# Performance work log

Hardware: AMD Instinct MI355X
Metric: run time of the kernel (lower is better)

Reference implementation:

```python
import jax, jax.numpy as jnp
import numpy as np

EPS = 1e-5
GROUPS = 32

def group_norm(x, w, b):
    B, C, H, W = x.shape
    g = GROUPS
    xr = x.reshape(B, g, C // g, H * W)
    mean = xr.mean(axis=(2, 3), keepdims=True)
    var = xr.var(axis=(2, 3), keepdims=True)
    h = ((xr - mean) / jnp.sqrt(var + EPS)).reshape(B, C, H, W)
    return h * w[None, :, None, None] + b[None, :, None, None]

def setup_inputs() -> dict:
    key = jax.random.key(0)
    ks = jax.random.split(key, 7)
    B, C, H, W = 8, 256, 64, 64
    d = C // 8  # 32
    x = jax.random.normal(ks[0], (B, C, H, W), dtype=jnp.float32)
    norm_w = 1.0 + 0.1 * jax.random.normal(ks[1], (C,), dtype=jnp.float32)
    norm_b = 0.1 * jax.random.normal(ks[2], (C,), dtype=jnp.float32)
    s = 1.0 / np.sqrt(C)
    Wq = jax.random.normal(ks[3], (d, C), dtype=jnp.float32) * s
    Wk = jax.random.normal(ks[4], (d, C), dtype=jnp.float32) * s
    Wv = jax.random.normal(ks[5], (C, C), dtype=jnp.float32) * s
    Wproj = jax.random.normal(ks[6], (C, C), dtype=jnp.float32) * s
    gamma = jnp.full((1,), 0.5, dtype=jnp.float32)  # torch init is 0; nonzero so attention path contributes
    return {"x": x, "norm_w": norm_w, "norm_b": norm_b, "Wq": Wq, "Wk": Wk,
            "Wv": Wv, "Wproj": Wproj, "gamma": gamma}

def reference(x, norm_w, norm_b, Wq, Wk, Wv, Wproj, gamma):
    B, C, H, W = x.shape
    N = H * W
    h = group_norm(x, norm_w, norm_b)           # (B,C,H,W)
    hf = h.reshape(B, C, N)                      # flatten spatial
    d = Wq.shape[0]
    q = jnp.einsum('dc,bcn->bnd', Wq, hf)        # (B,N,d)
    k = jnp.einsum('dc,bcn->bdn', Wk, hf)        # (B,d,N)
    v = jnp.einsum('oc,bcn->bno', Wv, hf)        # (B,N,C)
    scale = d ** (-0.5)
    attn = jax.nn.softmax(jnp.einsum('bnd,bdm->bnm', q, k) * scale, axis=-1)  # (B,N,N)
    out = jnp.einsum('bnm,bmo->bno', attn, v)    # (B,N,C)
    out = out.transpose(0, 2, 1).reshape(B, C, H, W)
    proj = jnp.einsum('oc,bchw->bohw', Wproj, out)
    return x + gamma[0] * proj
```

## Files before the change

kernel.cpp:

```cpp
#include <hip/hip_runtime.h>
#include <cstdint>


typedef __bf16 bf16x8 __attribute__((ext_vector_type(8)));
typedef float f32x4 __attribute__((ext_vector_type(4)));
typedef float f32x16 __attribute__((ext_vector_type(16)));
typedef unsigned int u32x4 __attribute__((ext_vector_type(4)));
typedef unsigned short u16x4 __attribute__((ext_vector_type(4)));
typedef unsigned short u16x8 __attribute__((ext_vector_type(8)));

#define DEVI __device__ __forceinline__

DEVI unsigned short f2bf(float f) {
    __bf16 h = (__bf16)f;
    return __builtin_bit_cast(unsigned short, h);
}
DEVI float bf2f(unsigned short u) {
    unsigned int x = ((unsigned int)u) << 16;
    return __builtin_bit_cast(float, x);
}

DEVI f32x4 mfma16(bf16x8 a, bf16x8 b, f32x4 c) {
    return __builtin_amdgcn_mfma_f32_16x16x32_bf16(a, b, c, 0, 0, 0);
}
DEVI f32x16 mfma32(bf16x8 a, bf16x8 b, f32x16 c) {
    return __builtin_amdgcn_mfma_f32_32x32x16_bf16(a, b, c, 0, 0, 0);
}

DEVI void glds16(const unsigned short* g, unsigned short* l) {
    const __attribute__((address_space(1))) unsigned int* gp =
        reinterpret_cast<const __attribute__((address_space(1))) unsigned int*>(
            reinterpret_cast<uintptr_t>(g));
    __attribute__((address_space(3))) unsigned int* lp =
        reinterpret_cast<__attribute__((address_space(3))) unsigned int*>(
            reinterpret_cast<uintptr_t>(l));
    __builtin_amdgcn_global_load_lds(gp, lp, 16, 0, 0);
}

DEVI void barrier_raw() {
    asm volatile("" ::: "memory");
    __builtin_amdgcn_s_barrier();
    asm volatile("" ::: "memory");
}
DEVI void wait_vm0() {
    __builtin_amdgcn_s_waitcnt(0x3F70);
}

#define QSCALE 0.2550663133f
#define MFIX   12.0f

__global__ __launch_bounds__(256) void k_pack(
        const float* __restrict__ wq, const float* __restrict__ wk,
        const float* __restrict__ wv, const float* __restrict__ wp,
        unsigned short* __restrict__ bqk, unsigned short* __restrict__ bv,
        unsigned short* __restrict__ bp) {
    int i = blockIdx.x * 256 + threadIdx.x;
    if (i < 8192)       bqk[i] = f2bf(wq[i] * QSCALE);
    else if (i < 16384) bqk[i] = f2bf(wk[i - 8192]);
    bv[i] = f2bf(wv[i]);
    bp[i] = f2bf(wp[i]);
}

__global__ __launch_bounds__(1024) void k_gnorm(
        const float* __restrict__ x, const float* __restrict__ gw,
        const float* __restrict__ gb, unsigned short* __restrict__ ht) {
    int bg = blockIdx.x;
    int b = bg >> 5, g = bg & 31;
    const float* xb = x + ((size_t)(b * 256 + g * 8)) * 4096;
    int t = threadIdx.x;
    float s1 = 0.f, s2 = 0.f;
    const f32x4* xv4 = (const f32x4*)xb;
    for (int i = t; i < 8192; i += 1024) {
        f32x4 v = xv4[i];
        #pragma unroll
        for (int j = 0; j < 4; j++) { s1 += v[j]; s2 += v[j] * v[j]; }
    }
    #pragma unroll
    for (int off = 1; off < 64; off <<= 1) {
        s1 += __shfl_xor(s1, off);
        s2 += __shfl_xor(s2, off);
    }
    __shared__ float red[34];
    int wv_ = t >> 6;
    if ((t & 63) == 0) { red[wv_ * 2] = s1; red[wv_ * 2 + 1] = s2; }
    __syncthreads();
    if (t == 0) {
        float a = 0.f, q = 0.f;
        #pragma unroll
        for (int i = 0; i < 16; i++) { a += red[i * 2]; q += red[i * 2 + 1]; }
        float mean = a * (1.f / 32768.f);
        float var = q * (1.f / 32768.f) - mean * mean;
        red[32] = mean; red[33] = rsqrtf(var + 1e-5f);
    }
    __syncthreads();
    float mean = red[32], rstd = red[33];
    float wv8[8], bv8[8];
    #pragma unroll
    for (int c = 0; c < 8; c++) { wv8[c] = gw[g * 8 + c] * rstd; bv8[c] = gb[g * 8 + c] - mean * rstd * gw[g * 8 + c]; }
    int n0 = t * 4;
    f32x4 cv[8];
    #pragma unroll
    for (int c = 0; c < 8; c++) cv[c] = *(const f32x4*)(xb + c * 4096 + n0);
    #pragma unroll
    for (int j = 0; j < 4; j++) {
        u16x8 pk;
        #pragma unroll
        for (int c = 0; c < 8; c++) pk[c] = f2bf(cv[c][j] * wv8[c] + bv8[c]);
        *(u16x8*)(&ht[((size_t)(b * 4096 + n0 + j)) * 256 + g * 8]) = pk;
    }
}

template <int EPI>
__global__ __launch_bounds__(256) void k_gemm(
        const unsigned short* __restrict__ A, const unsigned short* __restrict__ Bw,
        void* __restrict__ outp, const float* __restrict__ xres,
        const float* __restrict__ gamma, int ldout) {
    __shared__ unsigned short lA[128 * 72];
    __shared__ unsigned short lB[64 * 72];
    int t = threadIdx.x;
    int m0 = blockIdx.x * 128, n0 = blockIdx.y * 64;
    int w = t >> 6, lane = t & 63, l15 = lane & 15, quad = lane >> 4;
    f32x4 z4 = {0.f, 0.f, 0.f, 0.f};
    f32x4 acc[2][4];
    #pragma unroll
    for (int i = 0; i < 2; i++)
        #pragma unroll
        for (int j = 0; j < 4; j++) acc[i][j] = z4;

    for (int kb = 0; kb < 4; kb++) {
        #pragma unroll
        for (int i = 0; i < 4; i++) {
            int ch = i * 256 + t;
            int row = ch >> 3, col = (ch & 7) * 8;
            u32x4 v = *(const u32x4*)(A + (size_t)(m0 + row) * 256 + kb * 64 + col);
            *(u32x4*)(&lA[row * 72 + col]) = v;
        }
        #pragma unroll
        for (int i = 0; i < 2; i++) {
            int ch = i * 256 + t;
            int row = ch >> 3, col = (ch & 7) * 8;
            u32x4 v = *(const u32x4*)(Bw + (size_t)(n0 + row) * 256 + kb * 64 + col);
            *(u32x4*)(&lB[row * 72 + col]) = v;
        }
        __syncthreads();
        #pragma unroll
        for (int ks = 0; ks < 2; ks++) {
            bf16x8 af[2], bfr[4];
            #pragma unroll
            for (int fr = 0; fr < 2; fr++)
                af[fr] = *(const bf16x8*)(&lA[(w * 32 + fr * 16 + l15) * 72 + ks * 32 + quad * 8]);
            #pragma unroll
            for (int fn = 0; fn < 4; fn++)
                bfr[fn] = *(const bf16x8*)(&lB[(fn * 16 + l15) * 72 + ks * 32 + quad * 8]);
            #pragma unroll
            for (int fr = 0; fr < 2; fr++)
                #pragma unroll
                for (int fn = 0; fn < 4; fn++)
                    acc[fr][fn] = mfma16(af[fr], bfr[fn], acc[fr][fn]);
        }
        __syncthreads();
    }

    if (EPI == 0) {
        unsigned short* out = (unsigned short*)outp;
        #pragma unroll
        for (int fr = 0; fr < 2; fr++)
            #pragma unroll
            for (int fn = 0; fn < 4; fn++)
                #pragma unroll
                for (int r = 0; r < 4; r++) {
                    int m = m0 + w * 32 + fr * 16 + quad * 4 + r;
                    int n = n0 + fn * 16 + l15;
                    out[(size_t)m * ldout + n] = f2bf(acc[fr][fn][r]);
                }
    } else if (EPI == 1) {
        unsigned short* out = (unsigned short*)outp;
        int b = m0 >> 12, nb = (m0 & 4095) + w * 32;
        int swq = ((quad & 1) << 1) | (quad >> 1);
        #pragma unroll
        for (int fr = 0; fr < 2; fr++)
            #pragma unroll
            for (int fn = 0; fn < 4; fn++) {
                int o = n0 + fn * 16 + l15;
                int n = nb + fr * 16 + swq * 4;
                u16x4 pk;
                #pragma unroll
                for (int r = 0; r < 4; r++) pk[r] = f2bf(acc[fr][fn][r]);
                *(u16x4*)(&out[(((size_t)(b * 256 + o)) << 12) + n]) = pk;
            }
    } else {
        float* out = (float*)outp;
        float gm = gamma[0];
        int b = m0 >> 12, nb = (m0 & 4095) + w * 32;
        #pragma unroll
        for (int fr = 0; fr < 2; fr++)
            #pragma unroll
            for (int fn = 0; fn < 4; fn++) {
                int o = n0 + fn * 16 + l15;
                int n = nb + fr * 16 + quad * 4;
                size_t base = (((size_t)(b * 256 + o)) << 12) + n;
                f32x4 xv = *(const f32x4*)(xres + base);
                f32x4 ov;
                #pragma unroll
                for (int r = 0; r < 4; r++) ov[r] = xv[r] + gm * acc[fr][fn][r];
                *(f32x4*)(out + base) = ov;
            }
    }
}

__global__ __launch_bounds__(256, 2) void k_flash(
        const unsigned short* __restrict__ QK, const unsigned short* __restrict__ Vt,
        unsigned short* __restrict__ Oa) {
    __shared__ __align__(16) char smem[73728];
    int id = blockIdx.x;
    int b = id & 7, qt = id >> 3;
    int t = threadIdx.x, w = t >> 6, ln = t & 63;
    int l31 = ln & 31, h = ln >> 5;
    int qh = w >> 1, kh = w & 1;
    int q0 = qt * 64;

    const unsigned short* qrow = QK + ((size_t)(b * 4096 + q0 + qh * 32 + l31)) * 64;
    bf16x8 qb0 = *(const bf16x8*)(qrow + h * 8);
    bf16x8 qb1 = *(const bf16x8*)(qrow + 16 + h * 8);

    int cgK = (ln & 3) ^ ((ln >> 2) & 3) ^ ((ln >> 4) & 3);
    const unsigned short* gK = QK + ((size_t)(b * 4096 + w * 16 + (ln >> 2))) * 64 + 32 + cgK * 8;
    int vc8 = (ln & 7) ^ ((ln >> 3) & 7);
    const unsigned short* gV = Vt + (((size_t)(b * 256 + w * 64 + (ln >> 3))) << 12) + vc8 * 8;

    unsigned short* lK0 = (unsigned short*)smem;
    unsigned short* lV0 = (unsigned short*)(smem + 4096);
    unsigned short* lK1 = (unsigned short*)(smem + 36864);
    unsigned short* lV1 = (unsigned short*)(smem + 36864 + 4096);
    unsigned short* sK0 = lK0 + w * 512;
    unsigned short* sV0 = lV0 + w * 4096;
    unsigned short* sK1 = lK1 + w * 512;
    unsigned short* sV1 = lV1 + w * 4096;

    u16x8 onesu = {0x3F80, 0x3F80, 0x3F80, 0x3F80, 0x3F80, 0x3F80, 0x3F80, 0x3F80};
    bf16x8 ones = __builtin_bit_cast(bf16x8, onesu);
    f32x16 z16;
    #pragma unroll
    for (int i = 0; i < 16; i++) z16[i] = 0.f;
    f32x16 minit;
    #pragma unroll
    for (int i = 0; i < 16; i++) minit[i] = -MFIX;
    f32x16 Oacc[8];
    #pragma unroll
    for (int i = 0; i < 8; i++) Oacc[i] = z16;
    f32x16 lacc = z16;

    int gl = (l31 & 3) ^ ((l31 >> 2) & 3);
    const unsigned short* kf0p0 = lK0 + (kh * 32 + l31) * 32 + ((0 + h) ^ gl) * 8;
    const unsigned short* kf1p0 = lK0 + (kh * 32 + l31) * 32 + ((2 + h) ^ gl) * 8;
    const unsigned short* kf0p1 = lK1 + (kh * 32 + l31) * 32 + ((0 + h) ^ gl) * 8;
    const unsigned short* kf1p1 = lK1 + (kh * 32 + l31) * 32 + ((2 + h) ^ gl) * 8;
    int slotA = ((kh * 4 + 0 * 2 + h) ^ (ln & 7)) * 8;
    int slotB = ((kh * 4 + 1 * 2 + h) ^ (ln & 7)) * 8;

    auto stage = [&](int kn, unsigned short* sK, unsigned short* sV) {
        glds16(gK + (size_t)kn * 4096, sK);
        #pragma unroll
        for (int j = 0; j < 8; j++)
            glds16(gV + ((size_t)j * 8 << 12) + kn * 64, sV + j * 512);
    };

    auto compute = [&](const unsigned short* kf0p, const unsigned short* kf1p,
                       const unsigned short* lV) {
        bf16x8 kf0 = *(const bf16x8*)kf0p;
        bf16x8 kf1 = *(const bf16x8*)kf1p;
        f32x16 St = mfma32(kf0, qb0, minit);
        St = mfma32(kf1, qb1, St);
        u16x8 p0u, p1u;
        #pragma unroll
        for (int j = 0; j < 8; j++) {
            p0u[j] = f2bf(__builtin_amdgcn_exp2f(St[j]));
            p1u[j] = f2bf(__builtin_amdgcn_exp2f(St[8 + j]));
        }
        bf16x8 pa0 = __builtin_bit_cast(bf16x8, p0u);
        bf16x8 pa1 = __builtin_bit_cast(bf16x8, p1u);
        lacc = mfma32(pa0, ones, lacc);
        lacc = mfma32(pa1, ones, lacc);
        #pragma unroll
        for (int nt = 0; nt < 8; nt++) {
            bf16x8 vf = *(const bf16x8*)(lV + (nt * 32 + l31) * 64 + slotA);
            Oacc[nt] = mfma32(pa0, vf, Oacc[nt]);
        }
        #pragma unroll
        for (int nt = 0; nt < 8; nt++) {
            bf16x8 vf = *(const bf16x8*)(lV + (nt * 32 + l31) * 64 + slotB);
            Oacc[nt] = mfma32(pa1, vf, Oacc[nt]);
        }
    };

    stage(0, sK0, sV0);
    for (int kt = 0; kt < 64; kt += 2) {
        wait_vm0();
        barrier_raw();
        stage(kt + 1, sK1, sV1);
        compute(kf0p0, kf1p0, lV0);
        wait_vm0();
        barrier_raw();
        if (kt + 2 < 64) stage(kt + 2, sK0, sV0);
        compute(kf0p1, kf1p1, lV1);
    }
    __syncthreads();

    if (kh == 1) {
        #pragma unroll
        for (int nt = 0; nt < 8; nt++)
            #pragma unroll
            for (int rg = 0; rg < 2; rg++) {
                u16x8 pk;
                #pragma unroll
                for (int j = 0; j < 8; j++) pk[j] = f2bf(Oacc[nt][rg * 8 + j]);
                *(u16x8*)(smem + qh * 16384 + nt * 2048 + rg * 1024 + ln * 16) = pk;
            }
        #pragma unroll
        for (int rg = 0; rg < 4; rg++) {
            f32x4 lv;
            #pragma unroll
            for (int j = 0; j < 4; j++) lv[j] = lacc[rg * 4 + j];
            *(f32x4*)(smem + 32768 + qh * 4096 + rg * 1024 + ln * 16) = lv;
        }
    }
    __syncthreads();
    if (kh == 0) {
        float rl[16];
        #pragma unroll
        for (int rg = 0; rg < 4; rg++) {
            f32x4 lv = *(const f32x4*)(smem + 32768 + qh * 4096 + rg * 1024 + ln * 16);
            #pragma unroll
            for (int j = 0; j < 4; j++) rl[rg * 4 + j] = 1.f / (lacc[rg * 4 + j] + lv[j]);
        }
        size_t rb = (size_t)(b * 4096 + q0 + qh * 32);
        #pragma unroll
        for (int nt = 0; nt < 8; nt++)
            #pragma unroll
            for (int rg = 0; rg < 2; rg++) {
                u16x8 pk = *(const u16x8*)(smem + qh * 16384 + nt * 2048 + rg * 1024 + ln * 16);
                #pragma unroll
                for (int j = 0; j < 8; j++) {
                    int r = rg * 8 + j;
                    float val = (Oacc[nt][r] + bf2f(pk[j])) * rl[r];
                    int row = (r & 3) + 8 * (r >> 2) + 4 * h;
                    Oa[(rb + row) * 256 + nt * 32 + l31] = f2bf(val);
                }
            }
    }
}

extern "C" void kernel_launch(void* const* d_in, const int* in_sizes, int n_in,
                              void* d_out, int out_size, void* d_ws, size_t ws_size,
                              hipStream_t stream) {
    const float* x  = (const float*)d_in[0];
    const float* nw = (const float*)d_in[1];
    const float* nb = (const float*)d_in[2];
    const float* wq = (const float*)d_in[3];
    const float* wk = (const float*)d_in[4];
    const float* wv = (const float*)d_in[5];
    const float* wp = (const float*)d_in[6];
    const float* gm = (const float*)d_in[7];

    char* p = (char*)d_ws;
    unsigned short* ht  = (unsigned short*)p; p += (size_t)32768 * 256 * 2;
    unsigned short* qk  = (unsigned short*)p; p += (size_t)32768 * 64 * 2;
    unsigned short* vt  = (unsigned short*)p; p += (size_t)8 * 256 * 4096 * 2;
    unsigned short* oa  = (unsigned short*)p; p += (size_t)32768 * 256 * 2;
    unsigned short* bqk = (unsigned short*)p; p += 64 * 256 * 2;
    unsigned short* bv  = (unsigned short*)p; p += 256 * 256 * 2;
    unsigned short* bp  = (unsigned short*)p; p += 256 * 256 * 2;

    k_pack<<<dim3(256), dim3(256), 0, stream>>>(wq, wk, wv, wp, bqk, bv, bp);
    k_gnorm<<<dim3(256), dim3(1024), 0, stream>>>(x, nw, nb, ht);
    k_gemm<0><<<dim3(256, 1), dim3(256), 0, stream>>>(ht, bqk, (void*)qk, nullptr, nullptr, 64);
    k_gemm<1><<<dim3(256, 4), dim3(256), 0, stream>>>(ht, bv, (void*)vt, nullptr, nullptr, 0);
    k_flash<<<dim3(512), dim3(256), 0, stream>>>(qk, vt, oa);
    k_gemm<2><<<dim3(256, 4), dim3(256), 0, stream>>>(oa, bp, d_out, x, gm, 0);
}
```

Before: 234.4 us.

## Double query rows per flash block to reuse staged K/V tiles

Each flash-attention block now handles 128 query rows instead of 64, with each wave holding two 32-row query tiles and two sets of output accumulators. Every K/V tile staged into LDS is therefore used for twice as many queries, halving global K/V traffic and LDS reads per unit of work. The price is double the accumulator registers (occupancy bound lowered to one block per SIMD group), more LDS for the epilogue, and a grid cut to 256 blocks, which may underfill the GPU's compute units.

```diff
diff --git a/kernel.cpp b/kernel.cpp
--- a/kernel.cpp
+++ b/kernel.cpp
@@ -208,20 +208,24 @@
     }
 }
 
-__global__ __launch_bounds__(256, 2) void k_flash(
+__global__ __launch_bounds__(256, 1) void k_flash(
         const unsigned short* __restrict__ QK, const unsigned short* __restrict__ Vt,
         unsigned short* __restrict__ Oa) {
-    __shared__ __align__(16) char smem[73728];
+    __shared__ __align__(16) char smem[81920];
     int id = blockIdx.x;
     int b = id & 7, qt = id >> 3;
     int t = threadIdx.x, w = t >> 6, ln = t & 63;
     int l31 = ln & 31, h = ln >> 5;
     int qh = w >> 1, kh = w & 1;
-    int q0 = qt * 64;
-
-    const unsigned short* qrow = QK + ((size_t)(b * 4096 + q0 + qh * 32 + l31)) * 64;
-    bf16x8 qb0 = *(const bf16x8*)(qrow + h * 8);
-    bf16x8 qb1 = *(const bf16x8*)(qrow + 16 + h * 8);
+    int q0 = qt * 128 + qh * 64;
+
+    bf16x8 qb0[2], qb1[2];
+    #pragma unroll
+    for (int qt2 = 0; qt2 < 2; qt2++) {
+        const unsigned short* qrow = QK + ((size_t)(b * 4096 + q0 + qt2 * 32 + l31)) * 64;
+        qb0[qt2] = *(const bf16x8*)(qrow + h * 8);
+        qb1[qt2] = *(const bf16x8*)(qrow + 16 + h * 8);
+    }
 
     int cgK = (ln & 3) ^ ((ln >> 2) & 3) ^ ((ln >> 4) & 3);
     const unsigned short* gK = QK + ((size_t)(b * 4096 + w * 16 + (ln >> 2))) * 64 + 32 + cgK * 8;
@@ -245,10 +249,12 @@
     f32x16 minit;
     #pragma unroll
     for (int i = 0; i < 16; i++) minit[i] = -MFIX;
-    f32x16 Oacc[8];
-    #pragma unroll
-    for (int i = 0; i < 8; i++) Oacc[i] = z16;
-    f32x16 lacc = z16;
+    f32x16 Oacc[2][8];
+    #pragma unroll
+    for (int qt2 = 0; qt2 < 2; qt2++)
+        #pragma unroll
+        for (int i = 0; i < 8; i++) Oacc[qt2][i] = z16;
+    f32x16 lacc[2] = {z16, z16};
 
     int gl = (l31 & 3) ^ ((l31 >> 2) & 3);
     const unsigned short* kf0p0 = lK0 + (kh * 32 + l31) * 32 + ((0 + h) ^ gl) * 8;
@@ -269,27 +275,33 @@
                        const unsigned short* lV) {
         bf16x8 kf0 = *(const bf16x8*)kf0p;
         bf16x8 kf1 = *(const bf16x8*)kf1p;
-        f32x16 St = mfma32(kf0, qb0, minit);
-        St = mfma32(kf1, qb1, St);
-        u16x8 p0u, p1u;
-        #pragma unroll
-        for (int j = 0; j < 8; j++) {
-            p0u[j] = f2bf(__builtin_amdgcn_exp2f(St[j]));
-            p1u[j] = f2bf(__builtin_amdgcn_exp2f(St[8 + j]));
-        }
-        bf16x8 pa0 = __builtin_bit_cast(bf16x8, p0u);
-        bf16x8 pa1 = __builtin_bit_cast(bf16x8, p1u);
-        lacc = mfma32(pa0, ones, lacc);
-        lacc = mfma32(pa1, ones, lacc);
+        bf16x8 pa[2][2];
+        #pragma unroll
+        for (int qt2 = 0; qt2 < 2; qt2++) {
+            f32x16 St = mfma32(kf0, qb0[qt2], minit);
+            St = mfma32(kf1, qb1[qt2], St);
+            u16x8 p0u, p1u;
+            #pragma unroll
+            for (int j = 0; j < 8; j++) {
+                p0u[j] = f2bf(__builtin_amdgcn_exp2f(St[j]));
+                p1u[j] = f2bf(__builtin_amdgcn_exp2f(St[8 + j]));
+            }
+            pa[qt2][0] = __builtin_bit_cast(bf16x8, p0u);
+            pa[qt2][1] = __builtin_bit_cast(bf16x8, p1u);
+            lacc[qt2] = mfma32(pa[qt2][0], ones, lacc[qt2]);
+            lacc[qt2] = mfma32(pa[qt2][1], ones, lacc[qt2]);
+        }
         #pragma unroll
         for (int nt = 0; nt < 8; nt++) {
             bf16x8 vf = *(const bf16x8*)(lV + (nt * 32 + l31) * 64 + slotA);
-            Oacc[nt] = mfma32(pa0, vf, Oacc[nt]);
+            Oacc[0][nt] = mfma32(pa[0][0], vf, Oacc[0][nt]);
+            Oacc[1][nt] = mfma32(pa[1][0], vf, Oacc[1][nt]);
         }
         #pragma unroll
         for (int nt = 0; nt < 8; nt++) {
             bf16x8 vf = *(const bf16x8*)(lV + (nt * 32 + l31) * 64 + slotB);
-            Oacc[nt] = mfma32(pa1, vf, Oacc[nt]);
+            Oacc[0][nt] = mfma32(pa[0][1], vf, Oacc[0][nt]);
+            Oacc[1][nt] = mfma32(pa[1][1], vf, Oacc[1][nt]);
         }
     };
 
@@ -308,45 +320,51 @@
 
     if (kh == 1) {
         #pragma unroll
-        for (int nt = 0; nt < 8; nt++)
-            #pragma unroll
-            for (int rg = 0; rg < 2; rg++) {
-                u16x8 pk;
-                #pragma unroll
-                for (int j = 0; j < 8; j++) pk[j] = f2bf(Oacc[nt][rg * 8 + j]);
-                *(u16x8*)(smem + qh * 16384 + nt * 2048 + rg * 1024 + ln * 16) = pk;
-            }
-        #pragma unroll
-        for (int rg = 0; rg < 4; rg++) {
-            f32x4 lv;
-            #pragma unroll
-            for (int j = 0; j < 4; j++) lv[j] = lacc[rg * 4 + j];
-            *(f32x4*)(smem + 32768 + qh * 4096 + rg * 1024 + ln * 16) = lv;
+        for (int qt2 = 0; qt2 < 2; qt2++) {
+            #pragma unroll
+            for (int nt = 0; nt < 8; nt++)
+                #pragma unroll
+                for (int rg = 0; rg < 2; rg++) {
+                    u16x8 pk;
+                    #pragma unroll
+                    for (int j = 0; j < 8; j++) pk[j] = f2bf(Oacc[qt2][nt][rg * 8 + j]);
+                    *(u16x8*)(smem + qh * 32768 + qt2 * 16384 + nt * 2048 + rg * 1024 + ln * 16) = pk;
+                }
+            #pragma unroll
+            for (int rg = 0; rg < 4; rg++) {
+                f32x4 lv;
+                #pragma unroll
+                for (int j = 0; j < 4; j++) lv[j] = lacc[qt2][rg * 4 + j];
+                *(f32x4*)(smem + 65536 + qh * 8192 + qt2 * 4096 + rg * 1024 + ln * 16) = lv;
+            }
         }
     }
     __syncthreads();
     if (kh == 0) {
-        float rl[16];
-        #pragma unroll
-        for (int rg = 0; rg < 4; rg++) {
-            f32x4 lv = *(const f32x4*)(smem + 32768 + qh * 4096 + rg * 1024 + ln * 16);
-            #pragma unroll
-            for (int j = 0; j < 4; j++) rl[rg * 4 + j] = 1.f / (lacc[rg * 4 + j] + lv[j]);
-        }
-        size_t rb = (size_t)(b * 4096 + q0 + qh * 32);
-        #pragma unroll
-        for (int nt = 0; nt < 8; nt++)
-            #pragma unroll
-            for (int rg = 0; rg < 2; rg++) {
-                u16x8 pk = *(const u16x8*)(smem + qh * 16384 + nt * 2048 + rg * 1024 + ln * 16);
-                #pragma unroll
-                for (int j = 0; j < 8; j++) {
-                    int r = rg * 8 + j;
-                    float val = (Oacc[nt][r] + bf2f(pk[j])) * rl[r];
-                    int row = (r & 3) + 8 * (r >> 2) + 4 * h;
-                    Oa[(rb + row) * 256 + nt * 32 + l31] = f2bf(val);
+        #pragma unroll
+        for (int qt2 = 0; qt2 < 2; qt2++) {
+            float rl[16];
+            #pragma unroll
+            for (int rg = 0; rg < 4; rg++) {
+                f32x4 lv = *(const f32x4*)(smem + 65536 + qh * 8192 + qt2 * 4096 + rg * 1024 + ln * 16);
+                #pragma unroll
+                for (int j = 0; j < 4; j++) rl[rg * 4 + j] = 1.f / (lacc[qt2][rg * 4 + j] + lv[j]);
+            }
+            size_t rb = (size_t)(b * 4096 + qt * 128 + qh * 64 + qt2 * 32);
+            #pragma unroll
+            for (int nt = 0; nt < 8; nt++)
+                #pragma unroll
+                for (int rg = 0; rg < 2; rg++) {
+                    u16x8 pk = *(const u16x8*)(smem + qh * 32768 + qt2 * 16384 + nt * 2048 + rg * 1024 + ln * 16);
+                    #pragma unroll
+                    for (int j = 0; j < 8; j++) {
+                        int r = rg * 8 + j;
+                        float val = (Oacc[qt2][nt][r] + bf2f(pk[j])) * rl[r];
+                        int row = (r & 3) + 8 * (r >> 2) + 4 * h;
+                        Oa[(rb + row) * 256 + nt * 32 + l31] = f2bf(val);
+                    }
                 }
-            }
+        }
     }
 }
 
@@ -375,6 +393,6 @@
     k_gnorm<<<dim3(256), dim3(1024), 0, stream>>>(x, nw, nb, ht);
     k_gemm<0><<<dim3(256, 1), dim3(256), 0, stream>>>(ht, bqk, (void*)qk, nullptr, nullptr, 64);
     k_gemm<1><<<dim3(256, 4), dim3(256), 0, stream>>>(ht, bv, (void*)vt, nullptr, nullptr, 0);
-    k_flash<<<dim3(512), dim3(256), 0, stream>>>(qk, vt, oa);
+    k_flash<<<dim3(256), dim3(256), 0, stream>>>(qk, vt, oa);
     k_gemm<2><<<dim3(256, 4), dim3(256), 0, stream>>>(oa, bp, d_out, x, gm, 0);
 }
```

New measurement: 582.7 us. 149% more time.
